# Performance work log

Measured on AMD Instinct MI355X. Metric: run time of the kernel, lower is better.

## Reference

```python
import jax, jax.numpy as jnp
import numpy as np

EPS = 1e-8

def l2norm(x, axis=-1, eps=EPS):
    n = jnp.sqrt(jnp.sum(x * x, axis=axis, keepdims=True)) + eps
    return x / n

def setup_inputs() -> dict:
    key = jax.random.key(0)
    k1, k2, k3, k4 = jax.random.split(key, 4)
    B, Q, S, D, SIM = 512, 64, 36, 1024, 256
    query = jax.random.normal(k1, (B, Q, D), dtype=jnp.float32)
    context = jax.random.normal(k2, (B, S, D), dtype=jnp.float32)
    matrix = jax.random.uniform(k3, (B, Q, D), dtype=jnp.float32)
    W = jax.random.normal(k4, (SIM, D), dtype=jnp.float32) * 0.02
    b = jnp.zeros((SIM,), dtype=jnp.float32)
    return {"query": query, "context": context, "matrix": matrix,
            "W": W, "b": b, "smooth": 9}

def reference(query, context, matrix, W, b, smooth):
    # cross_attention
    q = query * matrix                                  # (B,Q,D)
    attn = jnp.einsum('bsd,bqd->bsq', context, q)       # (B,S,Q)
    attn = jnp.where(attn > 0, attn, 0.1 * attn)        # LeakyReLU(0.1)
    attn = l2norm(attn, axis=-1)                        # l2norm over Q
    attn = jnp.swapaxes(attn, 1, 2)                     # (B,Q,S)
    attn = jax.nn.softmax(attn * smooth, axis=2)        # temperature softmax over S
    wcontext = jnp.einsum('bqs,bsd->bqd', attn, context)
    wcontext = l2norm(wcontext, axis=-1)
    # Alignment_vector: squared diff -> linear -> l2norm
    sim_rep = (query - wcontext) ** 2                   # (B,Q,D)
    sim_rep = jnp.einsum('bqd,kd->bqk', sim_rep, W) + b # (B,Q,SIM)
    return l2norm(sim_rep, axis=-1)
```

## Files before the change

kernel.cpp:

```cpp
#include <hip/hip_runtime.h>
#include <hip/hip_bf16.h>

#define BB 512
#define QQ 64
#define SS 36
#define DD 1024
#define SIM 256

typedef unsigned short u16x8 __attribute__((ext_vector_type(8)));
typedef unsigned short u16x4 __attribute__((ext_vector_type(4)));
typedef __bf16 bf16x8 __attribute__((ext_vector_type(8)));
typedef float f32x4 __attribute__((ext_vector_type(4)));
typedef unsigned short us;

__device__ __forceinline__ us f2bf(float f) {
  unsigned u = __float_as_uint(f);
  u += 0x7FFFu + ((u >> 16) & 1u);
  return (us)(u >> 16);
}
__device__ __forceinline__ float bf2f(us h) {
  return __uint_as_float(((unsigned)h) << 16);
}

__global__ __launch_bounds__(256) void k0_w16(const float* __restrict__ W,
                                              us* __restrict__ W16) {
  int i = blockIdx.x * 256 + threadIdx.x;
  float4 v = ((const float4*)W)[i];
  ushort4 p;
  p.x = f2bf(v.x); p.y = f2bf(v.y); p.z = f2bf(v.z); p.w = f2bf(v.w);
  ((ushort4*)W16)[i] = p;
}

template <bool USE_W16>
__global__ __launch_bounds__(512, 4) void k_fused(
    const float* __restrict__ query, const float* __restrict__ context,
    const float* __restrict__ matrix, const float* __restrict__ Wm,
    const float* __restrict__ bvec, const int* __restrict__ smoothp,
    const us* __restrict__ W16, float* __restrict__ out) {
  __shared__ __align__(16) char smem[63232];
  us* qmL = (us*)smem;
  us* ctxL = (us*)(smem + 17408);
  float* sc = (float*)(smem + 30464);
  us* ctxTs = (us*)smem;
  us* A16s = (us*)(smem + 19456);
  us* P16s = (us*)(smem + 43520);
  us* Gf16L = (us*)(smem + 52736);
  float* biasL = (float*)(smem + 59648);
  float* rnL = (float*)(smem + 60672);
  float* rsum = (float*)(smem + 60928);

  const int t = threadIdx.x, bb = blockIdx.x;
  const int lane = t & 63, w = t >> 6;
  const int ml = lane & 15, kg = lane >> 4;
  const float smf = (float)smoothp[0];

  for (int idx = t; idx < 2304; idx += 512) ((unsigned*)P16s)[idx] = 0;
  for (int idx = t; idx < 1728; idx += 512) ((unsigned*)Gf16L)[idx] = 0;
  if (t < 256) biasL[t] = bvec[t];

  f32x4 acc[3], gacc[3];
#pragma unroll
  for (int j = 0; j < 3; ++j) {
    acc[j] = (f32x4){0.f, 0.f, 0.f, 0.f};
    gacc[j] = (f32x4){0.f, 0.f, 0.f, 0.f};
  }

  for (int ch = 0; ch < 8; ++ch) {
    const int d0 = ch * 128;
#pragma unroll
    for (int i = 0; i < 2; ++i) {
      int idx = t + 512 * i;
      int row = idx >> 4, c8 = idx & 15;
      const float4* gq = (const float4*)&query[((size_t)bb * QQ + row) * DD + d0 + c8 * 8];
      const float4* gm = (const float4*)&matrix[((size_t)bb * QQ + row) * DD + d0 + c8 * 8];
      float4 a0 = gq[0], a1 = gq[1], m0 = gm[0], m1 = gm[1];
      u16x8 pk;
      pk[0] = f2bf(a0.x * m0.x); pk[1] = f2bf(a0.y * m0.y);
      pk[2] = f2bf(a0.z * m0.z); pk[3] = f2bf(a0.w * m0.w);
      pk[4] = f2bf(a1.x * m1.x); pk[5] = f2bf(a1.y * m1.y);
      pk[6] = f2bf(a1.z * m1.z); pk[7] = f2bf(a1.w * m1.w);
      *(u16x8*)&qmL[row * 136 + c8 * 8] = pk;
    }
    {
      int row = t >> 4, c8 = t & 15;
      const float4* gc = (const float4*)&context[((size_t)bb * SS + row) * DD + d0 + c8 * 8];
      float4 a0 = gc[0], a1 = gc[1];
      u16x8 pk;
      pk[0] = f2bf(a0.x); pk[1] = f2bf(a0.y); pk[2] = f2bf(a0.z); pk[3] = f2bf(a0.w);
      pk[4] = f2bf(a1.x); pk[5] = f2bf(a1.y); pk[6] = f2bf(a1.z); pk[7] = f2bf(a1.w);
      *(u16x8*)&ctxL[row * 136 + c8 * 8] = pk;
    }
    if (t < 256) {
      int row = 32 + (t >> 4), c8 = t & 15;
      u16x8 pk = (u16x8){0, 0, 0, 0, 0, 0, 0, 0};
      if (row < 36) {
        const float4* gc = (const float4*)&context[((size_t)bb * SS + row) * DD + d0 + c8 * 8];
        float4 a0 = gc[0], a1 = gc[1];
        pk[0] = f2bf(a0.x); pk[1] = f2bf(a0.y); pk[2] = f2bf(a0.z); pk[3] = f2bf(a0.w);
        pk[4] = f2bf(a1.x); pk[5] = f2bf(a1.y); pk[6] = f2bf(a1.z); pk[7] = f2bf(a1.w);
      }
      *(u16x8*)&ctxL[row * 136 + c8 * 8] = pk;
    }
    __syncthreads();
#pragma unroll
    for (int ks = 0; ks < 4; ++ks) {
      const int ko = ks * 32 + kg * 8;
      if (w < 4) {
        bf16x8 bq = __builtin_bit_cast(bf16x8, *(const u16x8*)&qmL[(w * 16 + ml) * 136 + ko]);
#pragma unroll
        for (int mt = 0; mt < 3; ++mt) {
          bf16x8 af = __builtin_bit_cast(bf16x8, *(const u16x8*)&ctxL[(mt * 16 + ml) * 136 + ko]);
          acc[mt] = __builtin_amdgcn_mfma_f32_16x16x32_bf16(af, bq, acc[mt], 0, 0, 0);
        }
      } else if (w < 7) {
        bf16x8 ai = __builtin_bit_cast(bf16x8, *(const u16x8*)&ctxL[((w - 4) * 16 + ml) * 136 + ko]);
#pragma unroll
        for (int j = 0; j < 3; ++j) {
          bf16x8 aj = __builtin_bit_cast(bf16x8, *(const u16x8*)&ctxL[(j * 16 + ml) * 136 + ko]);
          gacc[j] = __builtin_amdgcn_mfma_f32_16x16x32_bf16(ai, aj, gacc[j], 0, 0, 0);
        }
      }
    }
    __syncthreads();
  }

  if (w < 4) {
#pragma unroll
    for (int mt = 0; mt < 3; ++mt)
#pragma unroll
      for (int ii = 0; ii < 4; ++ii) {
        float v = acc[mt][ii];
        v = v > 0.f ? v : 0.1f * v;
        sc[(mt * 16 + kg * 4 + ii) * 68 + w * 16 + ml] = v;
      }
  } else if (w < 7) {
#pragma unroll
    for (int j = 0; j < 3; ++j)
#pragma unroll
      for (int ii = 0; ii < 4; ++ii)
        Gf16L[((w - 4) * 16 + kg * 4 + ii) * 72 + j * 16 + ml] = f2bf(gacc[j][ii]);
  }
  __syncthreads();

  if (t < 36) {
    float ssum = 0.f;
    for (int qi = 0; qi < 64; ++qi) { float v = sc[t * 68 + qi]; ssum = fmaf(v, v, ssum); }
    float rn = 1.f / (sqrtf(ssum) + 1e-8f);
    for (int qi = 0; qi < 64; ++qi) sc[t * 68 + qi] *= rn;
  }
  __syncthreads();

  if (t < 64) {
    float mx = -1e30f;
    for (int s2 = 0; s2 < 36; ++s2) mx = fmaxf(mx, sc[s2 * 68 + t]);
    float sum = 0.f;
    float ev[36];
    for (int s2 = 0; s2 < 36; ++s2) {
      float e = __expf((sc[s2 * 68 + t] - mx) * smf);
      ev[s2] = e;
      sum += e;
    }
    float rs = 1.f / sum;
#pragma unroll
    for (int s2 = 0; s2 < 36; ++s2) P16s[t * 72 + s2] = f2bf(ev[s2] * rs);
  }
  __syncthreads();

  if (w < 3) {
    f32x4 accv[4];
#pragma unroll
    for (int mt = 0; mt < 4; ++mt) accv[mt] = (f32x4){0.f, 0.f, 0.f, 0.f};
#pragma unroll
    for (int ks = 0; ks < 2; ++ks) {
      const int ko = ks * 32 + kg * 8;
      bf16x8 gfr = __builtin_bit_cast(bf16x8, *(const u16x8*)&Gf16L[(w * 16 + ml) * 72 + ko]);
#pragma unroll
      for (int mt = 0; mt < 4; ++mt) {
        bf16x8 pf = __builtin_bit_cast(bf16x8, *(const u16x8*)&P16s[(mt * 16 + ml) * 72 + ko]);
        accv[mt] = __builtin_amdgcn_mfma_f32_16x16x32_bf16(pf, gfr, accv[mt], 0, 0, 0);
      }
    }
#pragma unroll
    for (int mt = 0; mt < 4; ++mt)
#pragma unroll
      for (int ii = 0; ii < 4; ++ii) {
        int q = mt * 16 + kg * 4 + ii;
        float vv = accv[mt][ii] * bf2f(P16s[q * 72 + w * 16 + ml]);
        vv += __shfl_xor(vv, 1);
        vv += __shfl_xor(vv, 2);
        vv += __shfl_xor(vv, 4);
        vv += __shfl_xor(vv, 8);
        if (ml == 0) rsum[q * 4 + w] = vv;
      }
  }
  __syncthreads();
  if (t < 64) {
    float s2 = rsum[t * 4] + rsum[t * 4 + 1] + rsum[t * 4 + 2];
    rnL[t] = 1.f / (sqrtf(s2) + 1e-8f);
  }
  for (int idx = t; idx < 1792; idx += 512) {
    int r = idx / 14, c = idx - r * 14;
    *(unsigned*)&ctxTs[r * 76 + 36 + c * 2] = 0;
  }
  __syncthreads();

  f32x4 accs[4][2];
#pragma unroll
  for (int mt = 0; mt < 4; ++mt)
#pragma unroll
    for (int ntl = 0; ntl < 2; ++ntl) accs[mt][ntl] = (f32x4){0.f, 0.f, 0.f, 0.f};

  for (int ch = 0; ch < 8; ++ch) {
    const int d0 = ch * 128;
    for (int idx = t; idx < 1152; idx += 512) {
      int d = idx & 127, s0 = (idx >> 7) * 4;
      const float* cp = &context[((size_t)bb * SS + s0) * DD + d0 + d];
      u16x4 pk;
      pk[0] = f2bf(cp[0]);
      pk[1] = f2bf(cp[DD]);
      pk[2] = f2bf(cp[2 * DD]);
      pk[3] = f2bf(cp[3 * DD]);
      *(u16x4*)&ctxTs[d * 76 + s0] = pk;
    }
    __syncthreads();
    f32x4 aw[4];
#pragma unroll
    for (int mt = 0; mt < 4; ++mt) aw[mt] = (f32x4){0.f, 0.f, 0.f, 0.f};
#pragma unroll
    for (int ks = 0; ks < 2; ++ks) {
      const int ko = ks * 32 + kg * 8;
      u16x4 blo = *(const u16x4*)&ctxTs[(w * 16 + ml) * 76 + ko];
      u16x4 bhi = *(const u16x4*)&ctxTs[(w * 16 + ml) * 76 + ko + 4];
      bf16x8 bfr = __builtin_bit_cast(bf16x8, __builtin_shufflevector(blo, bhi, 0, 1, 2, 3, 4, 5, 6, 7));
#pragma unroll
      for (int mt = 0; mt < 4; ++mt) {
        bf16x8 af = __builtin_bit_cast(bf16x8, *(const u16x8*)&P16s[(mt * 16 + ml) * 72 + ko]);
        aw[mt] = __builtin_amdgcn_mfma_f32_16x16x32_bf16(af, bfr, aw[mt], 0, 0, 0);
      }
    }
#pragma unroll
    for (int mt = 0; mt < 4; ++mt)
#pragma unroll
      for (int ii = 0; ii < 4; ++ii) {
        int q = mt * 16 + kg * 4 + ii;
        float qv = query[((size_t)bb * QQ + q) * DD + d0 + w * 16 + ml];
        float av = qv - aw[mt][ii] * rnL[q];
        A16s[q * 136 + w * 16 + ml] = f2bf(av * av);
      }
    __syncthreads();
#pragma unroll
    for (int ks = 0; ks < 4; ++ks) {
      const int ko = ks * 32 + kg * 8;
      bf16x8 bfr[2];
#pragma unroll
      for (int ntl = 0; ntl < 2; ++ntl) {
        const size_t wrow = (size_t)(w * 32 + ntl * 16 + ml);
        if constexpr (USE_W16) {
          bfr[ntl] = __builtin_bit_cast(bf16x8, *(const u16x8*)&W16[wrow * DD + d0 + ko]);
        } else {
          const float4* wp = (const float4*)&Wm[wrow * DD + d0 + ko];
          float4 x = wp[0], y = wp[1];
          u16x8 pk;
          pk[0] = f2bf(x.x); pk[1] = f2bf(x.y); pk[2] = f2bf(x.z); pk[3] = f2bf(x.w);
          pk[4] = f2bf(y.x); pk[5] = f2bf(y.y); pk[6] = f2bf(y.z); pk[7] = f2bf(y.w);
          bfr[ntl] = __builtin_bit_cast(bf16x8, pk);
        }
      }
#pragma unroll
      for (int mt = 0; mt < 4; ++mt) {
        bf16x8 af = __builtin_bit_cast(bf16x8, *(const u16x8*)&A16s[(mt * 16 + ml) * 136 + ko]);
#pragma unroll
        for (int ntl = 0; ntl < 2; ++ntl)
          accs[mt][ntl] = __builtin_amdgcn_mfma_f32_16x16x32_bf16(af, bfr[ntl], accs[mt][ntl], 0, 0, 0);
      }
    }
    __syncthreads();
  }

#pragma unroll
  for (int mt = 0; mt < 4; ++mt)
#pragma unroll
    for (int ii = 0; ii < 4; ++ii) {
      int q = mt * 16 + kg * 4 + ii;
      float partial = 0.f;
#pragma unroll
      for (int ntl = 0; ntl < 2; ++ntl) {
        int col = w * 32 + ntl * 16 + ml;
        float v = accs[mt][ntl][ii] + biasL[col];
        partial = fmaf(v, v, partial);
      }
      partial += __shfl_xor(partial, 1);
      partial += __shfl_xor(partial, 2);
      partial += __shfl_xor(partial, 4);
      partial += __shfl_xor(partial, 8);
      if (ml == 0) rsum[q * 9 + w] = partial;
    }
  __syncthreads();
  if (t < 64) {
    float ssum = 0.f;
#pragma unroll
    for (int w2 = 0; w2 < 8; ++w2) ssum += rsum[t * 9 + w2];
    rnL[t] = 1.f / (sqrtf(ssum) + 1e-8f);
  }
  __syncthreads();
#pragma unroll
  for (int mt = 0; mt < 4; ++mt)
#pragma unroll
    for (int ntl = 0; ntl < 2; ++ntl)
#pragma unroll
      for (int ii = 0; ii < 4; ++ii) {
        int q = mt * 16 + kg * 4 + ii;
        int col = w * 32 + ntl * 16 + ml;
        float v = accs[mt][ntl][ii] + biasL[col];
        out[((size_t)bb * QQ + q) * SIM + col] = v * rnL[q];
      }
}

extern "C" void kernel_launch(void* const* d_in, const int* in_sizes, int n_in,
                              void* d_out, int out_size, void* d_ws, size_t ws_size,
                              hipStream_t stream) {
  const float* query = (const float*)d_in[0];
  const float* context = (const float*)d_in[1];
  const float* matrix = (const float*)d_in[2];
  const float* Wm = (const float*)d_in[3];
  const float* bvec = (const float*)d_in[4];
  const int* smoothp = (const int*)d_in[5];
  float* out = (float*)d_out;

  us* W16 = (us*)d_ws;
  const bool useW16 = ws_size >= (size_t)SIM * DD * 2;

  if (useW16) {
    k0_w16<<<dim3(SIM * DD / 1024), dim3(256), 0, stream>>>(Wm, W16);
    k_fused<true><<<dim3(BB), dim3(512), 0, stream>>>(query, context, matrix, Wm,
                                                      bvec, smoothp, W16, out);
  } else {
    k_fused<false><<<dim3(BB), dim3(512), 0, stream>>>(query, context, matrix, Wm,
                                                       bvec, smoothp, W16, out);
  }
}
```

Baseline: 160.6 us.

## Keep full bf16 context resident in LDS and reuse it in second phase

The whole per-batch context (36x1024 bf16, padded to 48 rows) is now kept in a 150 KB dynamic LDS buffer during the first pass, so the second pass no longer reloads and transposes context from global memory. The weighted-context MFMA B operand is instead gathered column-wise from that buffer. Query is staged as bf16 in LDS rather than read with scalar global loads, and one trailing barrier is removed. The cost is much larger LDS use per block, which drops occupancy from four blocks to at most one per CU, plus strided LDS gathers and lower query precision.

```diff
diff --git a/kernel.cpp b/kernel.cpp
--- a/kernel.cpp
+++ b/kernel.cpp
@@ -8,7 +8,6 @@
 #define SIM 256
 
 typedef unsigned short u16x8 __attribute__((ext_vector_type(8)));
-typedef unsigned short u16x4 __attribute__((ext_vector_type(4)));
 typedef __bf16 bf16x8 __attribute__((ext_vector_type(8)));
 typedef float f32x4 __attribute__((ext_vector_type(4)));
 typedef unsigned short us;
@@ -31,29 +30,33 @@
   ((ushort4*)W16)[i] = p;
 }
 
+#define KF_LDS 153600
+
 template <bool USE_W16>
-__global__ __launch_bounds__(512, 4) void k_fused(
+__global__ __launch_bounds__(512, 2) void k_fused(
     const float* __restrict__ query, const float* __restrict__ context,
     const float* __restrict__ matrix, const float* __restrict__ Wm,
     const float* __restrict__ bvec, const int* __restrict__ smoothp,
     const us* __restrict__ W16, float* __restrict__ out) {
-  __shared__ __align__(16) char smem[63232];
-  us* qmL = (us*)smem;
-  us* ctxL = (us*)(smem + 17408);
-  float* sc = (float*)(smem + 30464);
-  us* ctxTs = (us*)smem;
-  us* A16s = (us*)(smem + 19456);
-  us* P16s = (us*)(smem + 43520);
-  us* Gf16L = (us*)(smem + 52736);
-  float* biasL = (float*)(smem + 59648);
-  float* rnL = (float*)(smem + 60672);
-  float* rsum = (float*)(smem + 60928);
+  extern __shared__ __align__(16) char smem[];
+  us* ctxL = (us*)smem;
+  us* qmL = (us*)(smem + 99072);
+  float* sc = (float*)(smem + 99072);
+  us* A16s = (us*)(smem + 99072);
+  us* qB = (us*)(smem + 116480);
+  us* P16s = (us*)(smem + 133888);
+  us* Gf16L = (us*)(smem + 143104);
+  float* biasL = (float*)(smem + 150016);
+  float* rnL = (float*)(smem + 151040);
+  float* rsum = (float*)(smem + 151296);
 
   const int t = threadIdx.x, bb = blockIdx.x;
   const int lane = t & 63, w = t >> 6;
   const int ml = lane & 15, kg = lane >> 4;
   const float smf = (float)smoothp[0];
 
+  for (int idx = t; idx < 6192; idx += 512)
+    ((unsigned*)(ctxL + 36 * 1032))[idx] = 0;
   for (int idx = t; idx < 2304; idx += 512) ((unsigned*)P16s)[idx] = 0;
   for (int idx = t; idx < 1728; idx += 512) ((unsigned*)Gf16L)[idx] = 0;
   if (t < 256) biasL[t] = bvec[t];
@@ -88,18 +91,16 @@
       u16x8 pk;
       pk[0] = f2bf(a0.x); pk[1] = f2bf(a0.y); pk[2] = f2bf(a0.z); pk[3] = f2bf(a0.w);
       pk[4] = f2bf(a1.x); pk[5] = f2bf(a1.y); pk[6] = f2bf(a1.z); pk[7] = f2bf(a1.w);
-      *(u16x8*)&ctxL[row * 136 + c8 * 8] = pk;
-    }
-    if (t < 256) {
+      *(u16x8*)&ctxL[row * 1032 + d0 + c8 * 8] = pk;
+    }
+    if (t < 64) {
       int row = 32 + (t >> 4), c8 = t & 15;
-      u16x8 pk = (u16x8){0, 0, 0, 0, 0, 0, 0, 0};
-      if (row < 36) {
-        const float4* gc = (const float4*)&context[((size_t)bb * SS + row) * DD + d0 + c8 * 8];
-        float4 a0 = gc[0], a1 = gc[1];
-        pk[0] = f2bf(a0.x); pk[1] = f2bf(a0.y); pk[2] = f2bf(a0.z); pk[3] = f2bf(a0.w);
-        pk[4] = f2bf(a1.x); pk[5] = f2bf(a1.y); pk[6] = f2bf(a1.z); pk[7] = f2bf(a1.w);
-      }
-      *(u16x8*)&ctxL[row * 136 + c8 * 8] = pk;
+      const float4* gc = (const float4*)&context[((size_t)bb * SS + row) * DD + d0 + c8 * 8];
+      float4 a0 = gc[0], a1 = gc[1];
+      u16x8 pk;
+      pk[0] = f2bf(a0.x); pk[1] = f2bf(a0.y); pk[2] = f2bf(a0.z); pk[3] = f2bf(a0.w);
+      pk[4] = f2bf(a1.x); pk[5] = f2bf(a1.y); pk[6] = f2bf(a1.z); pk[7] = f2bf(a1.w);
+      *(u16x8*)&ctxL[row * 1032 + d0 + c8 * 8] = pk;
     }
     __syncthreads();
 #pragma unroll
@@ -109,14 +110,17 @@
         bf16x8 bq = __builtin_bit_cast(bf16x8, *(const u16x8*)&qmL[(w * 16 + ml) * 136 + ko]);
 #pragma unroll
         for (int mt = 0; mt < 3; ++mt) {
-          bf16x8 af = __builtin_bit_cast(bf16x8, *(const u16x8*)&ctxL[(mt * 16 + ml) * 136 + ko]);
+          bf16x8 af = __builtin_bit_cast(
+              bf16x8, *(const u16x8*)&ctxL[(mt * 16 + ml) * 1032 + d0 + ko]);
           acc[mt] = __builtin_amdgcn_mfma_f32_16x16x32_bf16(af, bq, acc[mt], 0, 0, 0);
         }
       } else if (w < 7) {
-        bf16x8 ai = __builtin_bit_cast(bf16x8, *(const u16x8*)&ctxL[((w - 4) * 16 + ml) * 136 + ko]);
+        bf16x8 ai = __builtin_bit_cast(
+            bf16x8, *(const u16x8*)&ctxL[((w - 4) * 16 + ml) * 1032 + d0 + ko]);
 #pragma unroll
         for (int j = 0; j < 3; ++j) {
-          bf16x8 aj = __builtin_bit_cast(bf16x8, *(const u16x8*)&ctxL[(j * 16 + ml) * 136 + ko]);
+          bf16x8 aj = __builtin_bit_cast(
+              bf16x8, *(const u16x8*)&ctxL[(j * 16 + ml) * 1032 + d0 + ko]);
           gacc[j] = __builtin_amdgcn_mfma_f32_16x16x32_bf16(ai, aj, gacc[j], 0, 0, 0);
         }
       }
@@ -198,10 +202,6 @@
     float s2 = rsum[t * 4] + rsum[t * 4 + 1] + rsum[t * 4 + 2];
     rnL[t] = 1.f / (sqrtf(s2) + 1e-8f);
   }
-  for (int idx = t; idx < 1792; idx += 512) {
-    int r = idx / 14, c = idx - r * 14;
-    *(unsigned*)&ctxTs[r * 76 + 36 + c * 2] = 0;
-  }
   __syncthreads();
 
   f32x4 accs[4][2];
@@ -212,38 +212,50 @@
 
   for (int ch = 0; ch < 8; ++ch) {
     const int d0 = ch * 128;
-    for (int idx = t; idx < 1152; idx += 512) {
-      int d = idx & 127, s0 = (idx >> 7) * 4;
-      const float* cp = &context[((size_t)bb * SS + s0) * DD + d0 + d];
-      u16x4 pk;
-      pk[0] = f2bf(cp[0]);
-      pk[1] = f2bf(cp[DD]);
-      pk[2] = f2bf(cp[2 * DD]);
-      pk[3] = f2bf(cp[3 * DD]);
-      *(u16x4*)&ctxTs[d * 76 + s0] = pk;
+#pragma unroll
+    for (int i = 0; i < 2; ++i) {
+      int idx = t + 512 * i;
+      int row = idx >> 4, c8 = idx & 15;
+      const float4* gq = (const float4*)&query[((size_t)bb * QQ + row) * DD + d0 + c8 * 8];
+      float4 a0 = gq[0], a1 = gq[1];
+      u16x8 pk;
+      pk[0] = f2bf(a0.x); pk[1] = f2bf(a0.y); pk[2] = f2bf(a0.z); pk[3] = f2bf(a0.w);
+      pk[4] = f2bf(a1.x); pk[5] = f2bf(a1.y); pk[6] = f2bf(a1.z); pk[7] = f2bf(a1.w);
+      *(u16x8*)&qB[row * 136 + c8 * 8] = pk;
+    }
+    f32x4 aw[4];
+#pragma unroll
+    for (int mt = 0; mt < 4; ++mt) aw[mt] = (f32x4){0.f, 0.f, 0.f, 0.f};
+    {
+      const int ncol = d0 + w * 16 + ml;
+      u16x8 g0;
+#pragma unroll
+      for (int j = 0; j < 8; ++j) g0[j] = ctxL[(kg * 8 + j) * 1032 + ncol];
+      bf16x8 bfr0 = __builtin_bit_cast(bf16x8, g0);
+#pragma unroll
+      for (int mt = 0; mt < 4; ++mt) {
+        bf16x8 af = __builtin_bit_cast(bf16x8, *(const u16x8*)&P16s[(mt * 16 + ml) * 72 + kg * 8]);
+        aw[mt] = __builtin_amdgcn_mfma_f32_16x16x32_bf16(af, bfr0, aw[mt], 0, 0, 0);
+      }
+      u16x8 g1;
+#pragma unroll
+      for (int j = 0; j < 8; ++j)
+        g1[j] = (kg < 2) ? ctxL[(32 + kg * 8 + j) * 1032 + ncol] : (us)0;
+      bf16x8 bfr1 = __builtin_bit_cast(bf16x8, g1);
+#pragma unroll
+      for (int mt = 0; mt < 4; ++mt) {
+        bf16x8 af =
+            __builtin_bit_cast(bf16x8, *(const u16x8*)&P16s[(mt * 16 + ml) * 72 + 32 + kg * 8]);
+        aw[mt] = __builtin_amdgcn_mfma_f32_16x16x32_bf16(af, bfr1, aw[mt], 0, 0, 0);
+      }
     }
     __syncthreads();
-    f32x4 aw[4];
-#pragma unroll
-    for (int mt = 0; mt < 4; ++mt) aw[mt] = (f32x4){0.f, 0.f, 0.f, 0.f};
-#pragma unroll
-    for (int ks = 0; ks < 2; ++ks) {
-      const int ko = ks * 32 + kg * 8;
-      u16x4 blo = *(const u16x4*)&ctxTs[(w * 16 + ml) * 76 + ko];
-      u16x4 bhi = *(const u16x4*)&ctxTs[(w * 16 + ml) * 76 + ko + 4];
-      bf16x8 bfr = __builtin_bit_cast(bf16x8, __builtin_shufflevector(blo, bhi, 0, 1, 2, 3, 4, 5, 6, 7));
-#pragma unroll
-      for (int mt = 0; mt < 4; ++mt) {
-        bf16x8 af = __builtin_bit_cast(bf16x8, *(const u16x8*)&P16s[(mt * 16 + ml) * 72 + ko]);
-        aw[mt] = __builtin_amdgcn_mfma_f32_16x16x32_bf16(af, bfr, aw[mt], 0, 0, 0);
-      }
-    }
 #pragma unroll
     for (int mt = 0; mt < 4; ++mt)
 #pragma unroll
       for (int ii = 0; ii < 4; ++ii) {
         int q = mt * 16 + kg * 4 + ii;
-        float qv = query[((size_t)bb * QQ + q) * DD + d0 + w * 16 + ml];
+        float qv = bf2f(qB[q * 136 + w * 16 + ml]);
         float av = qv - aw[mt][ii] * rnL[q];
         A16s[q * 136 + w * 16 + ml] = f2bf(av * av);
       }
@@ -271,11 +283,12 @@
         bf16x8 af = __builtin_bit_cast(bf16x8, *(const u16x8*)&A16s[(mt * 16 + ml) * 136 + ko]);
 #pragma unroll
         for (int ntl = 0; ntl < 2; ++ntl)
-          accs[mt][ntl] = __builtin_amdgcn_mfma_f32_16x16x32_bf16(af, bfr[ntl], accs[mt][ntl], 0, 0, 0);
-      }
-    }
-    __syncthreads();
-  }
+          accs[mt][ntl] =
+              __builtin_amdgcn_mfma_f32_16x16x32_bf16(af, bfr[ntl], accs[mt][ntl], 0, 0, 0);
+      }
+    }
+  }
+  __syncthreads();
 
 #pragma unroll
   for (int mt = 0; mt < 4; ++mt)
@@ -330,12 +343,17 @@
   us* W16 = (us*)d_ws;
   const bool useW16 = ws_size >= (size_t)SIM * DD * 2;
 
+  hipFuncSetAttribute((const void*)k_fused<true>,
+                      hipFuncAttributeMaxDynamicSharedMemorySize, KF_LDS);
+  hipFuncSetAttribute((const void*)k_fused<false>,
+                      hipFuncAttributeMaxDynamicSharedMemorySize, KF_LDS);
+
   if (useW16) {
     k0_w16<<<dim3(SIM * DD / 1024), dim3(256), 0, stream>>>(Wm, W16);
-    k_fused<true><<<dim3(BB), dim3(512), 0, stream>>>(query, context, matrix, Wm,
-                                                      bvec, smoothp, W16, out);
+    k_fused<true><<<dim3(BB), dim3(512), KF_LDS, stream>>>(query, context, matrix, Wm,
+                                                           bvec, smoothp, W16, out);
   } else {
-    k_fused<false><<<dim3(BB), dim3(512), 0, stream>>>(query, context, matrix, Wm,
-                                                       bvec, smoothp, W16, out);
-  }
-}
+    k_fused<false><<<dim3(BB), dim3(512), KF_LDS, stream>>>(query, context, matrix, Wm,
+                                                            bvec, smoothp, W16, out);
+  }
+}
```

Measured after the change: 151.2 us. 1.06x faster.

## Cache query in registers during phase one and shrink shared memory overlay

Applied to the files above, without the earlier changes.

Loads the query values needed by the squared-difference stage during the first chunk loop and keeps them as packed bf16 in registers, removing the second global read of query. Shared memory buffers are overlaid to reduce LDS footprint, context padding rows are zeroed once up front, and both chunk loops are fully unrolled. This raises register pressure and rounds query to bf16 before the subtraction, slightly changing numerics.

```diff
diff --git a/kernel.cpp b/kernel.cpp
--- a/kernel.cpp
+++ b/kernel.cpp
@@ -37,26 +37,32 @@
     const float* __restrict__ matrix, const float* __restrict__ Wm,
     const float* __restrict__ bvec, const int* __restrict__ smoothp,
     const us* __restrict__ W16, float* __restrict__ out) {
-  __shared__ __align__(16) char smem[63232];
-  us* qmL = (us*)smem;
-  us* ctxL = (us*)(smem + 17408);
-  float* sc = (float*)(smem + 30464);
+  __shared__ __align__(16) char smem[56576];
+  us* ctxA = (us*)smem;
   us* ctxTs = (us*)smem;
+  us* qmA = (us*)(smem + 19456);
+  float* sc = (float*)(smem + 19456);
   us* A16s = (us*)(smem + 19456);
-  us* P16s = (us*)(smem + 43520);
-  us* Gf16L = (us*)(smem + 52736);
-  float* biasL = (float*)(smem + 59648);
-  float* rnL = (float*)(smem + 60672);
-  float* rsum = (float*)(smem + 60928);
+  us* P16s = (us*)(smem + 36864);
+  us* Gf16L = (us*)(smem + 46080);
+  float* biasL = (float*)(smem + 52992);
+  float* rnL = (float*)(smem + 54016);
+  float* rsum = (float*)(smem + 54272);
 
   const int t = threadIdx.x, bb = blockIdx.x;
   const int lane = t & 63, w = t >> 6;
   const int ml = lane & 15, kg = lane >> 4;
   const float smf = (float)smoothp[0];
 
+  for (int idx = t; idx < 816; idx += 512)
+    ((unsigned*)(ctxA + 36 * 136))[idx] = 0;
   for (int idx = t; idx < 2304; idx += 512) ((unsigned*)P16s)[idx] = 0;
   for (int idx = t; idx < 1728; idx += 512) ((unsigned*)Gf16L)[idx] = 0;
   if (t < 256) biasL[t] = bvec[t];
+  __syncthreads();
+
+  u16x8 qr0[8], qr1[8];
+  const float* qcol = query + (size_t)bb * QQ * DD + w * 16 + ml;
 
   f32x4 acc[3], gacc[3];
 #pragma unroll
@@ -65,6 +71,7 @@
     gacc[j] = (f32x4){0.f, 0.f, 0.f, 0.f};
   }
 
+#pragma unroll
   for (int ch = 0; ch < 8; ++ch) {
     const int d0 = ch * 128;
 #pragma unroll
@@ -79,7 +86,7 @@
       pk[2] = f2bf(a0.z * m0.z); pk[3] = f2bf(a0.w * m0.w);
       pk[4] = f2bf(a1.x * m1.x); pk[5] = f2bf(a1.y * m1.y);
       pk[6] = f2bf(a1.z * m1.z); pk[7] = f2bf(a1.w * m1.w);
-      *(u16x8*)&qmL[row * 136 + c8 * 8] = pk;
+      *(u16x8*)&qmA[row * 136 + c8 * 8] = pk;
     }
     {
       int row = t >> 4, c8 = t & 15;
@@ -88,38 +95,57 @@
       u16x8 pk;
       pk[0] = f2bf(a0.x); pk[1] = f2bf(a0.y); pk[2] = f2bf(a0.z); pk[3] = f2bf(a0.w);
       pk[4] = f2bf(a1.x); pk[5] = f2bf(a1.y); pk[6] = f2bf(a1.z); pk[7] = f2bf(a1.w);
-      *(u16x8*)&ctxL[row * 136 + c8 * 8] = pk;
-    }
-    if (t < 256) {
+      *(u16x8*)&ctxA[row * 136 + c8 * 8] = pk;
+    }
+    if (t < 64) {
       int row = 32 + (t >> 4), c8 = t & 15;
-      u16x8 pk = (u16x8){0, 0, 0, 0, 0, 0, 0, 0};
-      if (row < 36) {
-        const float4* gc = (const float4*)&context[((size_t)bb * SS + row) * DD + d0 + c8 * 8];
-        float4 a0 = gc[0], a1 = gc[1];
-        pk[0] = f2bf(a0.x); pk[1] = f2bf(a0.y); pk[2] = f2bf(a0.z); pk[3] = f2bf(a0.w);
-        pk[4] = f2bf(a1.x); pk[5] = f2bf(a1.y); pk[6] = f2bf(a1.z); pk[7] = f2bf(a1.w);
-      }
-      *(u16x8*)&ctxL[row * 136 + c8 * 8] = pk;
+      const float4* gc = (const float4*)&context[((size_t)bb * SS + row) * DD + d0 + c8 * 8];
+      float4 a0 = gc[0], a1 = gc[1];
+      u16x8 pk;
+      pk[0] = f2bf(a0.x); pk[1] = f2bf(a0.y); pk[2] = f2bf(a0.z); pk[3] = f2bf(a0.w);
+      pk[4] = f2bf(a1.x); pk[5] = f2bf(a1.y); pk[6] = f2bf(a1.z); pk[7] = f2bf(a1.w);
+      *(u16x8*)&ctxA[row * 136 + c8 * 8] = pk;
+    }
+    float sv[16];
+    {
+#pragma unroll
+      for (int j = 0; j < 16; ++j) {
+        int q = (j >> 2) * 16 + kg * 4 + (j & 3);
+        sv[j] = qcol[(size_t)q * DD + d0];
+      }
     }
     __syncthreads();
 #pragma unroll
     for (int ks = 0; ks < 4; ++ks) {
       const int ko = ks * 32 + kg * 8;
       if (w < 4) {
-        bf16x8 bq = __builtin_bit_cast(bf16x8, *(const u16x8*)&qmL[(w * 16 + ml) * 136 + ko]);
+        bf16x8 bq = __builtin_bit_cast(bf16x8, *(const u16x8*)&qmA[(w * 16 + ml) * 136 + ko]);
 #pragma unroll
         for (int mt = 0; mt < 3; ++mt) {
-          bf16x8 af = __builtin_bit_cast(bf16x8, *(const u16x8*)&ctxL[(mt * 16 + ml) * 136 + ko]);
+          bf16x8 af = __builtin_bit_cast(
+              bf16x8, *(const u16x8*)&ctxA[(mt * 16 + ml) * 136 + ko]);
           acc[mt] = __builtin_amdgcn_mfma_f32_16x16x32_bf16(af, bq, acc[mt], 0, 0, 0);
         }
       } else if (w < 7) {
-        bf16x8 ai = __builtin_bit_cast(bf16x8, *(const u16x8*)&ctxL[((w - 4) * 16 + ml) * 136 + ko]);
+        bf16x8 ai = __builtin_bit_cast(
+            bf16x8, *(const u16x8*)&ctxA[((w - 4) * 16 + ml) * 136 + ko]);
 #pragma unroll
         for (int j = 0; j < 3; ++j) {
-          bf16x8 aj = __builtin_bit_cast(bf16x8, *(const u16x8*)&ctxL[(j * 16 + ml) * 136 + ko]);
+          bf16x8 aj = __builtin_bit_cast(
+              bf16x8, *(const u16x8*)&ctxA[(j * 16 + ml) * 136 + ko]);
           gacc[j] = __builtin_amdgcn_mfma_f32_16x16x32_bf16(ai, aj, gacc[j], 0, 0, 0);
         }
       }
+    }
+    {
+      u16x8 s0, s1;
+#pragma unroll
+      for (int j = 0; j < 8; ++j) {
+        s0[j] = f2bf(sv[j]);
+        s1[j] = f2bf(sv[8 + j]);
+      }
+      qr0[ch] = s0;
+      qr1[ch] = s1;
     }
     __syncthreads();
   }
@@ -193,15 +219,15 @@
         if (ml == 0) rsum[q * 4 + w] = vv;
       }
   }
+  for (int idx = t; idx < 1792; idx += 512) {
+    int r = idx / 14, c = idx - r * 14;
+    *(unsigned*)&ctxTs[r * 76 + 36 + c * 2] = 0;
+  }
   __syncthreads();
   if (t < 64) {
     float s2 = rsum[t * 4] + rsum[t * 4 + 1] + rsum[t * 4 + 2];
     rnL[t] = 1.f / (sqrtf(s2) + 1e-8f);
   }
-  for (int idx = t; idx < 1792; idx += 512) {
-    int r = idx / 14, c = idx - r * 14;
-    *(unsigned*)&ctxTs[r * 76 + 36 + c * 2] = 0;
-  }
   __syncthreads();
 
   f32x4 accs[4][2];
@@ -210,6 +236,7 @@
 #pragma unroll
     for (int ntl = 0; ntl < 2; ++ntl) accs[mt][ntl] = (f32x4){0.f, 0.f, 0.f, 0.f};
 
+#pragma unroll
   for (int ch = 0; ch < 8; ++ch) {
     const int d0 = ch * 128;
     for (int idx = t; idx < 1152; idx += 512) {
@@ -231,7 +258,8 @@
       const int ko = ks * 32 + kg * 8;
       u16x4 blo = *(const u16x4*)&ctxTs[(w * 16 + ml) * 76 + ko];
       u16x4 bhi = *(const u16x4*)&ctxTs[(w * 16 + ml) * 76 + ko + 4];
-      bf16x8 bfr = __builtin_bit_cast(bf16x8, __builtin_shufflevector(blo, bhi, 0, 1, 2, 3, 4, 5, 6, 7));
+      bf16x8 bfr = __builtin_bit_cast(
+          bf16x8, __builtin_shufflevector(blo, bhi, 0, 1, 2, 3, 4, 5, 6, 7));
 #pragma unroll
       for (int mt = 0; mt < 4; ++mt) {
         bf16x8 af = __builtin_bit_cast(bf16x8, *(const u16x8*)&P16s[(mt * 16 + ml) * 72 + ko]);
@@ -243,7 +271,8 @@
 #pragma unroll
       for (int ii = 0; ii < 4; ++ii) {
         int q = mt * 16 + kg * 4 + ii;
-        float qv = query[((size_t)bb * QQ + q) * DD + d0 + w * 16 + ml];
+        const int e = mt * 4 + ii;
+        float qv = bf2f(e < 8 ? qr0[ch][e] : qr1[ch][e - 8]);
         float av = qv - aw[mt][ii] * rnL[q];
         A16s[q * 136 + w * 16 + ml] = f2bf(av * av);
       }
@@ -271,7 +300,8 @@
         bf16x8 af = __builtin_bit_cast(bf16x8, *(const u16x8*)&A16s[(mt * 16 + ml) * 136 + ko]);
 #pragma unroll
         for (int ntl = 0; ntl < 2; ++ntl)
-          accs[mt][ntl] = __builtin_amdgcn_mfma_f32_16x16x32_bf16(af, bfr[ntl], accs[mt][ntl], 0, 0, 0);
+          accs[mt][ntl] =
+              __builtin_amdgcn_mfma_f32_16x16x32_bf16(af, bfr[ntl], accs[mt][ntl], 0, 0, 0);
       }
     }
     __syncthreads();
```

Measured after the change: 180.7 us. 1.12x slower.
